# Kernel tuning notes

Measured on AMD Instinct MI355X. Metric: run time of the kernel, lower is better.

The kernel has to match this reference:

```python
import jax, jax.numpy as jnp
import numpy as np

NEG_INF = -1e8  # masked_fill value from the torch code
EPS_DICE = 0.001
EPS_DIV = 1e-5
LOSS_FACTOR = 1.0  # loss['factor']


def conv2d(x, w, b, pad):
    # x: [B,C,H,W], w: [O,I,kh,kw] (OIHW), b: [O]
    y = jax.lax.conv_general_dilated(
        x, w, window_strides=(1, 1), padding=[(pad, pad), (pad, pad)],
        dimension_numbers=("NCHW", "OIHW", "NCHW"))
    return y + b[None, :, None, None]


def setup_inputs() -> dict:
    key = jax.random.key(0)
    ks = jax.random.split(key, 12)
    B, C, H, W = 2, 256, 64, 64
    s = 0.05  # small init scale to keep logits in a sane range
    inp = {
        "feats": jax.random.normal(ks[0], (B, C, H, W), jnp.float32),
        "masks": jax.random.randint(ks[1], (B, H, W), 0, 2).astype(jnp.float32),
        "layouts": jax.random.randint(ks[2], (B, H, W), 0, 16).astype(jnp.int32),
        "w_pre0": jax.random.normal(ks[3], (C, C, 3, 3), jnp.float32) * s,
        "b_pre0": jax.random.normal(ks[4], (C,), jnp.float32) * s,
        "w_pre1": jax.random.normal(ks[5], (C, C, 3, 3), jnp.float32) * s,
        "b_pre1": jax.random.normal(ks[6], (C,), jnp.float32) * s,
        "w_kernel": jax.random.normal(ks[7], (C + 1, C, 1, 1), jnp.float32) * s,
        "b_kernel": jax.random.normal(ks[8], (C + 1,), jnp.float32) * s,
        "w_feats": jax.random.normal(ks[9], (C, C, 1, 1), jnp.float32) * s,
        "b_feats": jax.random.normal(ks[10], (C,), jnp.float32) * s,
    }
    return inp


def reference(feats, masks, layouts, w_pre0, b_pre0, w_pre1, b_pre1,
              w_kernel, b_kernel, w_feats, b_feats):
    B, C, H, W = feats.shape
    # pre_kernel_convs: two 3x3 conv + ReLU
    h = jax.nn.relu(conv2d(feats, w_pre0, b_pre0, pad=1))
    h = jax.nn.relu(conv2d(h, w_pre1, b_pre1, pad=1))
    kernels = conv2d(h, w_kernel, b_kernel, pad=0)          # [B, C+1, H, W]
    f = conv2d(feats, w_feats, b_feats, pad=0)               # [B, C,   H, W]
    # permute(0,2,3,1).reshape(B, H*W, C+1): per-cell dynamic 1x1 conv params
    kernels = kernels.transpose(0, 2, 3, 1).reshape(B, H * W, C + 1)
    kw = kernels[..., :C]                                    # [B, P, C]
    kb = kernels[..., C]                                     # [B, P]
    # grouped 1x1 conv == batched matmul over channel dim
    logits = jnp.einsum("bpc,bchw->bphw", kw, f) + kb[:, :, None, None]
    logits = jnp.where(masks[:, None, :, :] > 0, logits, NEG_INF)  # [B,P,H,W]

    # --- training loss (dice, div='all') ---
    # segm_labels[b, r*W+c] = (layouts[b] == layouts[b,r,c])
    flat = layouts.reshape(B, H * W)
    labels = (layouts[:, None, :, :] == flat[:, :, None, None]).astype(logits.dtype)
    p = jax.nn.sigmoid(logits)
    d = 2.0 * (p * labels) / (p * p + EPS_DICE + labels * labels + EPS_DICE)
    loss_el = 1.0 - d                                        # [B, P, H, W]
    m_flat = masks.reshape(B, H * W)
    num = ((loss_el * masks[:, None, :, :]).sum((-1, -2)) * m_flat).sum(-1)  # [B]
    grid = masks.sum((1, 2))
    loss = (LOSS_FACTOR * num / (grid * grid + EPS_DIV)).mean()
    return logits, loss
```

## Files before the change

kernel.cpp:

```cpp
#include <hip/hip_runtime.h>
#include <hip/hip_bf16.h>
#include <math.h>

typedef __attribute__((ext_vector_type(8))) short bf16x8;
typedef __attribute__((ext_vector_type(4))) float f32x4;
typedef __hip_bfloat16 bf16_t;

#define NEG_INF_V -100000000.0f

__device__ __forceinline__ void gload16(const void* g, void* l) {
  __builtin_amdgcn_global_load_lds(
      (const __attribute__((address_space(1))) unsigned int*)g,
      (__attribute__((address_space(3))) unsigned int*)l, 16, 0, 0);
}

__device__ __forceinline__ bf16x8 swzread(const short* base, int r, int c) {
  return *(const bf16x8*)(base + ((r * 8 + (c ^ (r & 7))) << 3));
}

__global__ __launch_bounds__(256) void pad_cast_k(
    const float* __restrict__ feats, bf16_t* __restrict__ x_pad) {
  __shared__ float s[64][65];
  const int t = threadIdx.x;
  const int y = blockIdx.x, c0 = blockIdx.y * 64, b = blockIdx.z;
  bf16_t* xp = x_pad + (size_t)b * (66 * 66 * 256) + (size_t)y * 66 * 256 + c0;
  if (y == 0 || y == 65) {
    for (int i = t; i < 66 * 64; i += 256) {
      int px = i >> 6, ci = i & 63;
      xp[(size_t)px * 256 + ci] = __float2bfloat16(0.f);
    }
    return;
  }
  const float* fb = feats + ((size_t)b * 256 + c0) * 4096 + (size_t)(y - 1) * 64;
  for (int i = t; i < 64 * 64; i += 256) {
    int ci = i >> 6, x = i & 63;
    s[ci][x] = fb[(size_t)ci * 4096 + x];
  }
  __syncthreads();
  if (t < 128) {
    int px = (t >> 6) * 65, ci = t & 63;
    xp[(size_t)px * 256 + ci] = __float2bfloat16(0.f);
  }
  for (int i = t; i < 64 * 64; i += 256) {
    int xi = i >> 6, ci = i & 63;
    xp[(size_t)(xi + 1) * 256 + ci] = __float2bfloat16(s[ci][xi]);
  }
}

__global__ __launch_bounds__(256) void castw_all_k(
    const float* __restrict__ w0, const float* __restrict__ w1,
    const float* __restrict__ wk, const float* __restrict__ wf,
    bf16_t* __restrict__ o0, bf16_t* __restrict__ o1,
    bf16_t* __restrict__ ok, bf16_t* __restrict__ of) {
  const int bid = blockIdx.x, t = threadIdx.x;
  if (bid < 512) {
    int which = bid >> 8, co = bid & 255;
    const float* ws = which ? w1 : w0;
    bf16_t* wd = which ? o1 : o0;
#pragma unroll
    for (int k = 0; k < 9; ++k)
      wd[(size_t)co * 2304 + k * 256 + t] = __float2bfloat16(ws[((size_t)co * 256 + t) * 9 + k]);
  } else {
    int i = (bid - 512) * 256 + t;
    if (i < 257 * 256) ok[i] = __float2bfloat16(wk[i]);
    else { int j = i - 257 * 256; if (j < 256 * 256) of[j] = __float2bfloat16(wf[j]); }
  }
}

__global__ __launch_bounds__(256) void conv3x3_mfma_k(
    const bf16_t* __restrict__ xpad, const bf16_t* __restrict__ wr,
    const float* __restrict__ bias, bf16_t* __restrict__ out,
    int out_row_stride, int out_base, long out_bstride) {
  __shared__ __align__(16) short ldsA[2][8192];
  __shared__ __align__(16) short ldsB[2][8192];
  const int t = threadIdx.x, w = t >> 6, lane = t & 63;
  const int y = blockIdx.x, co0 = blockIdx.y * 64, b = blockIdx.z;
  const bf16_t* xb = xpad + (size_t)b * (66 * 66 * 256);
  const int wm = w >> 1, wn = w & 1;
  f32x4 acc[2][2] = {};

  int arow[4], akh[4], alsl[4];
#pragma unroll
  for (int pp = 0; pp < 4; ++pp) {
    int u = (pp * 4 + w) * 64 + lane;
    int gr = u >> 3, slot = u & 7;
    arow[pp] = gr & 63; akh[pp] = gr >> 6;
    alsl[pp] = (slot ^ (gr & 7)) * 8;
  }
  const int fr = lane & 15, fc = lane >> 4;

  auto stage = [&](int ks, int buf) {
    int kpos = ks >> 1, ck0 = (ks & 1) * 128;
    int ky = (kpos * 11) >> 5, kx = kpos - 3 * ky;
#pragma unroll
    for (int pp = 0; pp < 4; ++pp) {
      gload16(xb + ((size_t)(y + ky) * 66 + arow[pp] + kx) * 256 + kpos * 0 + ck0 + akh[pp] * 64 + alsl[pp]
                 + (size_t)kpos * 0,
              &ldsA[buf][(pp * 4 + w) * 512]);
      gload16(wr + (size_t)(co0 + arow[pp]) * 2304 + kpos * 256 + ck0 + akh[pp] * 64 + alsl[pp],
              &ldsB[buf][(pp * 4 + w) * 512]);
    }
  };
  auto compute = [&](int buf) {
#pragma unroll
    for (int kk = 0; kk < 4; ++kk) {
      const short* bA = &ldsA[buf][(kk >> 1) * 4096];
      const short* bB = &ldsB[buf][(kk >> 1) * 4096];
      int c = (kk & 1) * 4 + fc;
      bf16x8 af[2], bfr[2];
#pragma unroll
      for (int m = 0; m < 2; ++m) af[m] = swzread(bA, wm * 32 + m * 16 + fr, c);
#pragma unroll
      for (int n = 0; n < 2; ++n) bfr[n] = swzread(bB, wn * 32 + n * 16 + fr, c);
#pragma unroll
      for (int m = 0; m < 2; ++m)
#pragma unroll
        for (int n = 0; n < 2; ++n)
          acc[m][n] = __builtin_amdgcn_mfma_f32_16x16x32_bf16(af[m], bfr[n], acc[m][n], 0, 0, 0);
    }
  };

  stage(0, 0);
  __syncthreads();
  for (int ks = 0; ks < 17; ++ks) {
    stage(ks + 1, (ks + 1) & 1);
    compute(ks & 1);
    __syncthreads();
  }
  compute(1);

  bf16_t* ob = out + (size_t)b * out_bstride;
  float bv[2];
#pragma unroll
  for (int n = 0; n < 2; ++n) bv[n] = bias[co0 + wn * 32 + n * 16 + fr];
#pragma unroll
  for (int m = 0; m < 2; ++m)
#pragma unroll
    for (int r = 0; r < 4; ++r) {
      int x = wm * 32 + m * 16 + fc * 4 + r;
      size_t ra = (size_t)out_base + (size_t)y * out_row_stride + (size_t)x * 256 + co0 + wn * 32 + fr;
#pragma unroll
      for (int n = 0; n < 2; ++n) {
        float v = acc[m][n][r] + bv[n];
        ob[ra + n * 16] = __float2bfloat16(fmaxf(v, 0.f));
      }
    }
}

template <bool KER>
__global__ __launch_bounds__(256) void conv1x1_mfma_k(
    const bf16_t* __restrict__ in, const bf16_t* __restrict__ wt,
    const float* __restrict__ bias, bf16_t* __restrict__ outw,
    float* __restrict__ outkb, int A0, int AS, long in_bstride, int comax) {
  __shared__ __align__(16) short ldsA[16384];
  __shared__ __align__(16) short ldsB[16384];
  const int t = threadIdx.x, w = t >> 6, lane = t & 63;
  const int y = blockIdx.x, co0 = blockIdx.y * 64, b = blockIdx.z;
  const bf16_t* inb = in + (size_t)b * in_bstride;
  const int wm = w >> 1, wn = w & 1;
  f32x4 acc[2][2] = {};
  const int fr = lane & 15, fc = lane >> 4;

#pragma unroll
  for (int pp = 0; pp < 8; ++pp) {
    int u = (pp * 4 + w) * 64 + lane;
    int gr = u >> 3, slot = u & 7;
    int row = gr & 63, kh = gr >> 6;
    int lsl = (slot ^ (gr & 7)) * 8;
    gload16(inb + (size_t)A0 + (size_t)y * AS + (size_t)row * 256 + kh * 64 + lsl,
            &ldsA[(pp * 4 + w) * 512]);
    gload16(wt + (size_t)min(co0 + row, comax - 1) * 256 + kh * 64 + lsl,
            &ldsB[(pp * 4 + w) * 512]);
  }
  __syncthreads();
#pragma unroll
  for (int kk = 0; kk < 8; ++kk) {
    const short* bA = &ldsA[(kk >> 1) * 4096];
    const short* bB = &ldsB[(kk >> 1) * 4096];
    int c = (kk & 1) * 4 + fc;
    bf16x8 af[2], bfr[2];
#pragma unroll
    for (int m = 0; m < 2; ++m) af[m] = swzread(bA, wm * 32 + m * 16 + fr, c);
#pragma unroll
    for (int n = 0; n < 2; ++n) bfr[n] = swzread(bB, wn * 32 + n * 16 + fr, c);
#pragma unroll
    for (int m = 0; m < 2; ++m)
#pragma unroll
      for (int n = 0; n < 2; ++n)
        acc[m][n] = __builtin_amdgcn_mfma_f32_16x16x32_bf16(af[m], bfr[n], acc[m][n], 0, 0, 0);
  }

#pragma unroll
  for (int m = 0; m < 2; ++m)
#pragma unroll
    for (int r = 0; r < 4; ++r) {
      int x = wm * 32 + m * 16 + fc * 4 + r;
      int prow = y * 64 + x;
#pragma unroll
      for (int n = 0; n < 2; ++n) {
        int co = co0 + wn * 32 + n * 16 + fr;
        float v = acc[m][n][r] + bias[min(co, comax - 1)];
        if (KER) {
          if (co < 256) outw[((size_t)b * 4096 + prow) * 256 + co] = __float2bfloat16(v);
          else if (co == 256) outkb[(size_t)b * 4096 + prow] = v;
        } else {
          outw[((size_t)b * 4096 + prow) * 256 + co] = __float2bfloat16(v);
        }
      }
    }
}

__global__ __launch_bounds__(256) void logits_mfma_k(
    const bf16_t* __restrict__ kwt, const float* __restrict__ kb,
    const bf16_t* __restrict__ fft, const float* __restrict__ masks,
    const int* __restrict__ layouts, float* __restrict__ out,
    float* __restrict__ partial) {
  __shared__ __align__(16) short ldsA[2][8192];
  __shared__ __align__(16) short ldsB[2][8192];
  const int t = threadIdx.x, w = t >> 6, lane = t & 63;
  const int p0 = blockIdx.x * 128, q0 = blockIdx.y * 128, b = blockIdx.z;
  const bf16_t* ab = kwt + (size_t)b * (4096 * 256);
  const bf16_t* bb = fft + (size_t)b * (4096 * 256);
  const int wm = w >> 1, wn = w & 1;
  f32x4 acc[4][4] = {};

  int grow[4], glsl[4];
#pragma unroll
  for (int pp = 0; pp < 4; ++pp) {
    int u = (pp * 4 + w) * 64 + lane;
    int gr = u >> 3, slot = u & 7;
    grow[pp] = gr;
    glsl[pp] = (slot ^ (gr & 7)) * 8;
  }
  const int fr = lane & 15, fc = lane >> 4;

  auto stage = [&](int ks, int buf) {
    int cik = ks * 64;
#pragma unroll
    for (int pp = 0; pp < 4; ++pp) {
      gload16(ab + (size_t)(p0 + grow[pp]) * 256 + cik + glsl[pp], &ldsA[buf][(pp * 4 + w) * 512]);
      gload16(bb + (size_t)(q0 + grow[pp]) * 256 + cik + glsl[pp], &ldsB[buf][(pp * 4 + w) * 512]);
    }
  };
  auto compute = [&](int buf) {
#pragma unroll
    for (int kk = 0; kk < 2; ++kk) {
      int c = kk * 4 + fc;
      bf16x8 af[4], bfr[4];
#pragma unroll
      for (int m = 0; m < 4; ++m) af[m] = swzread(ldsA[buf], wm * 64 + m * 16 + fr, c);
#pragma unroll
      for (int n = 0; n < 4; ++n) bfr[n] = swzread(ldsB[buf], wn * 64 + n * 16 + fr, c);
#pragma unroll
      for (int m = 0; m < 4; ++m)
#pragma unroll
        for (int n = 0; n < 4; ++n)
          acc[m][n] = __builtin_amdgcn_mfma_f32_16x16x32_bf16(af[m], bfr[n], acc[m][n], 0, 0, 0);
    }
  };

  stage(0, 0);
  __syncthreads();
  for (int ks = 0; ks < 3; ++ks) {
    stage(ks + 1, (ks + 1) & 1);
    compute(ks & 1);
    __syncthreads();
  }
  compute(1);

  float mq[4];
  int layq[4];
#pragma unroll
  for (int n = 0; n < 4; ++n) {
    int q = q0 + wn * 64 + n * 16 + fr;
    mq[n] = masks[b * 4096 + q];
    layq[n] = layouts[b * 4096 + q];
  }
  float sl[16];
#pragma unroll
  for (int i = 0; i < 16; ++i) sl[i] = 0.f;
  float* outb = out + (size_t)b * 4096 * 4096;
#pragma unroll
  for (int m = 0; m < 4; ++m) {
#pragma unroll
    for (int r = 0; r < 4; ++r) {
      int p = p0 + wm * 64 + m * 16 + fc * 4 + r;
      float kbv = kb[b * 4096 + p];
      int layp = layouts[b * 4096 + p];
      float s = 0.f;
      size_t ra = (size_t)p * 4096 + q0 + wn * 64 + fr;
#pragma unroll
      for (int n = 0; n < 4; ++n) {
        float lg = (mq[n] > 0.f) ? (acc[m][n][r] + kbv) : NEG_INF_V;
        outb[ra + n * 16] = lg;
        float pz = 1.f / (1.f + __expf(-lg));
        float lab = (layp == layq[n]) ? 1.f : 0.f;
        float d = 2.f * pz * lab / (pz * pz + lab + 0.002f);
        s += (1.f - d) * mq[n];
      }
      sl[m * 4 + r] = s;
    }
  }
#pragma unroll
  for (int i = 0; i < 16; ++i) {
    float v = sl[i];
    v += __shfl_xor(v, 1); v += __shfl_xor(v, 2);
    v += __shfl_xor(v, 4); v += __shfl_xor(v, 8);
    sl[i] = v;
  }
  if (fr == 0) {
    int qt = blockIdx.y * 2 + wn;
#pragma unroll
    for (int m = 0; m < 4; ++m)
#pragma unroll
      for (int r = 0; r < 4; ++r) {
        int p = p0 + wm * 64 + m * 16 + fc * 4 + r;
        partial[((size_t)b * 4096 + p) * 64 + qt] = sl[m * 4 + r];
      }
  }
}

__global__ __launch_bounds__(256) void rowsum_k(
    const float* __restrict__ partial, const float* __restrict__ masks,
    float* __restrict__ accum) {
  const int t = threadIdx.x, w = t >> 6, lane = t & 63;
  const int idx = blockIdx.x * 256 + t;
  const int b = idx >> 12;
  const float* pp = partial + (size_t)idx * 64;
  float s = 0.f;
#pragma unroll
  for (int k = 0; k < 64; ++k) s += pp[k];
  float mp = masks[idx];
  float num = s * mp;
#pragma unroll
  for (int off = 32; off; off >>= 1) {
    num += __shfl_down(num, off);
    mp += __shfl_down(mp, off);
  }
  __shared__ float sn[4], sm[4];
  if (lane == 0) { sn[w] = num; sm[w] = mp; }
  __syncthreads();
  if (t == 0) {
    atomicAdd(&accum[b * 2], sn[0] + sn[1] + sn[2] + sn[3]);
    atomicAdd(&accum[b * 2 + 1], sm[0] + sm[1] + sm[2] + sm[3]);
  }
}

__global__ void loss_final_k(const float* __restrict__ accum, float* __restrict__ out_loss) {
  if (threadIdx.x == 0) {
    float l0 = accum[0] / (accum[1] * accum[1] + 1e-5f);
    float l1 = accum[2] / (accum[3] * accum[3] + 1e-5f);
    out_loss[0] = 0.5f * (l0 + l1);
  }
}

extern "C" void kernel_launch(void* const* d_in, const int* in_sizes, int n_in,
                              void* d_out, int out_size, void* d_ws, size_t ws_size,
                              hipStream_t stream) {
  const float* feats = (const float*)d_in[0];
  const float* masks = (const float*)d_in[1];
  const int* layouts = (const int*)d_in[2];
  const float* w_pre0 = (const float*)d_in[3];
  const float* b_pre0 = (const float*)d_in[4];
  const float* w_pre1 = (const float*)d_in[5];
  const float* b_pre1 = (const float*)d_in[6];
  const float* w_kernel = (const float*)d_in[7];
  const float* b_kernel = (const float*)d_in[8];
  const float* w_feats = (const float*)d_in[9];
  const float* b_feats = (const float*)d_in[10];

  bf16_t* x_pad = (bf16_t*)d_ws;
  bf16_t* h1p = x_pad + 2 * 1115136;
  bf16_t* h2 = h1p + 2 * 1115136;
  bf16_t* w0r = h2 + 2 * 1048576;
  bf16_t* w1r = w0r + 589824;
  bf16_t* wkb = w1r + 589824;
  bf16_t* wfb = wkb + 65792;
  bf16_t* kwt = wfb + 65536;
  bf16_t* fft = kwt + 2 * 1048576;
  float* kb = (float*)(fft + 2 * 1048576);
  float* partial = kb + 8192;
  float* accum = partial + 524288;
  float* out = (float*)d_out;

  hipMemsetAsync(h1p, 0, (size_t)2 * 1115136 * sizeof(bf16_t), stream);
  hipMemsetAsync(accum, 0, 4 * sizeof(float), stream);

  pad_cast_k<<<dim3(66, 4, 2), 256, 0, stream>>>(feats, x_pad);
  castw_all_k<<<dim3(1026), 256, 0, stream>>>(w_pre0, w_pre1, w_kernel, w_feats,
                                              w0r, w1r, wkb, wfb);

  conv3x3_mfma_k<<<dim3(64, 4, 2), 256, 0, stream>>>(
      x_pad, w0r, b_pre0, h1p, 66 * 256, 67 * 256, 1115136L);
  conv3x3_mfma_k<<<dim3(64, 4, 2), 256, 0, stream>>>(
      h1p, w1r, b_pre1, h2, 64 * 256, 0, 1048576L);

  conv1x1_mfma_k<true><<<dim3(64, 5, 2), 256, 0, stream>>>(
      h2, wkb, b_kernel, kwt, kb, 0, 16384, 1048576L, 257);
  conv1x1_mfma_k<false><<<dim3(64, 4, 2), 256, 0, stream>>>(
      x_pad, wfb, b_feats, fft, nullptr, 67 * 256, 66 * 256, 1115136L, 256);

  logits_mfma_k<<<dim3(32, 32, 2), 256, 0, stream>>>(
      kwt, kb, fft, masks, layouts, out, partial);

  rowsum_k<<<dim3(32), 256, 0, stream>>>(partial, masks, accum);
  loss_final_k<<<1, 64, 0, stream>>>(accum, out + (size_t)2 * 4096 * 4096);
}
```

Before: 293.6 us.

## Stage logits tile through LDS for coalesced float4 stores and simplify dice math

The logits epilogue now writes each 64x128 half-tile into shared memory, reusing the GEMM staging buffer, and then stores it to global memory as row-contiguous float4 writes instead of scattered 4-byte stores. The dice term is rewritten algebraically: it is computed from exp(-lg) with one reciprocal, only label-matching entries are accumulated, and the row total is mqsum minus that sum. This targets the 134 MB logits output write, which dominates traffic. It adds extra syncthreads and serialises the two warp-row halves, and the exp is clamped to avoid overflow.

```diff
diff --git a/kernel.cpp b/kernel.cpp
--- a/kernel.cpp
+++ b/kernel.cpp
@@ -94,8 +94,7 @@
     int ky = (kpos * 11) >> 5, kx = kpos - 3 * ky;
 #pragma unroll
     for (int pp = 0; pp < 4; ++pp) {
-      gload16(xb + ((size_t)(y + ky) * 66 + arow[pp] + kx) * 256 + kpos * 0 + ck0 + akh[pp] * 64 + alsl[pp]
-                 + (size_t)kpos * 0,
+      gload16(xb + ((size_t)(y + ky) * 66 + arow[pp] + kx) * 256 + ck0 + akh[pp] * 64 + alsl[pp],
               &ldsA[buf][(pp * 4 + w) * 512]);
       gload16(wr + (size_t)(co0 + arow[pp]) * 2304 + kpos * 256 + ck0 + akh[pp] * 64 + alsl[pp],
               &ldsB[buf][(pp * 4 + w) * 512]);
@@ -215,8 +214,10 @@
     const bf16_t* __restrict__ fft, const float* __restrict__ masks,
     const int* __restrict__ layouts, float* __restrict__ out,
     float* __restrict__ partial) {
-  __shared__ __align__(16) short ldsA[2][8192];
-  __shared__ __align__(16) short ldsB[2][8192];
+  __shared__ __align__(16) short ldsbuf[32768];
+  short* ldsA0 = ldsbuf;
+  short* ldsB0 = ldsbuf + 16384;
+  float* ldsf = (float*)ldsbuf;
   const int t = threadIdx.x, w = t >> 6, lane = t & 63;
   const int p0 = blockIdx.x * 128, q0 = blockIdx.y * 128, b = blockIdx.z;
   const bf16_t* ab = kwt + (size_t)b * (4096 * 256);
@@ -238,8 +239,10 @@
     int cik = ks * 64;
 #pragma unroll
     for (int pp = 0; pp < 4; ++pp) {
-      gload16(ab + (size_t)(p0 + grow[pp]) * 256 + cik + glsl[pp], &ldsA[buf][(pp * 4 + w) * 512]);
-      gload16(bb + (size_t)(q0 + grow[pp]) * 256 + cik + glsl[pp], &ldsB[buf][(pp * 4 + w) * 512]);
+      gload16(ab + (size_t)(p0 + grow[pp]) * 256 + cik + glsl[pp],
+              &ldsA0[buf * 8192 + (pp * 4 + w) * 512]);
+      gload16(bb + (size_t)(q0 + grow[pp]) * 256 + cik + glsl[pp],
+              &ldsB0[buf * 8192 + (pp * 4 + w) * 512]);
     }
   };
   auto compute = [&](int buf) {
@@ -248,9 +251,9 @@
       int c = kk * 4 + fc;
       bf16x8 af[4], bfr[4];
 #pragma unroll
-      for (int m = 0; m < 4; ++m) af[m] = swzread(ldsA[buf], wm * 64 + m * 16 + fr, c);
-#pragma unroll
-      for (int n = 0; n < 4; ++n) bfr[n] = swzread(ldsB[buf], wn * 64 + n * 16 + fr, c);
+      for (int m = 0; m < 4; ++m) af[m] = swzread(&ldsA0[buf * 8192], wm * 64 + m * 16 + fr, c);
+#pragma unroll
+      for (int n = 0; n < 4; ++n) bfr[n] = swzread(&ldsB0[buf * 8192], wn * 64 + n * 16 + fr, c);
 #pragma unroll
       for (int m = 0; m < 4; ++m)
 #pragma unroll
@@ -276,31 +279,51 @@
     mq[n] = masks[b * 4096 + q];
     layq[n] = layouts[b * 4096 + q];
   }
+  float mqsum = mq[0] + mq[1] + mq[2] + mq[3];
+  mqsum += __shfl_xor(mqsum, 1); mqsum += __shfl_xor(mqsum, 2);
+  mqsum += __shfl_xor(mqsum, 4); mqsum += __shfl_xor(mqsum, 8);
+
   float sl[16];
-#pragma unroll
-  for (int i = 0; i < 16; ++i) sl[i] = 0.f;
   float* outb = out + (size_t)b * 4096 * 4096;
-#pragma unroll
-  for (int m = 0; m < 4; ++m) {
-#pragma unroll
-    for (int r = 0; r < 4; ++r) {
-      int p = p0 + wm * 64 + m * 16 + fc * 4 + r;
-      float kbv = kb[b * 4096 + p];
-      int layp = layouts[b * 4096 + p];
-      float s = 0.f;
-      size_t ra = (size_t)p * 4096 + q0 + wn * 64 + fr;
-#pragma unroll
-      for (int n = 0; n < 4; ++n) {
-        float lg = (mq[n] > 0.f) ? (acc[m][n][r] + kbv) : NEG_INF_V;
-        outb[ra + n * 16] = lg;
-        float pz = 1.f / (1.f + __expf(-lg));
-        float lab = (layp == layq[n]) ? 1.f : 0.f;
-        float d = 2.f * pz * lab / (pz * pz + lab + 0.002f);
-        s += (1.f - d) * mq[n];
+  __syncthreads();
+
+  for (int half = 0; half < 2; ++half) {
+    if (wm == half) {
+#pragma unroll
+      for (int m = 0; m < 4; ++m) {
+#pragma unroll
+        for (int r = 0; r < 4; ++r) {
+          int pl = m * 16 + fc * 4 + r;
+          int p = p0 + wm * 64 + pl;
+          float kbv = kb[b * 4096 + p];
+          int layp = layouts[b * 4096 + p];
+          float dsum = 0.f;
+#pragma unroll
+          for (int n = 0; n < 4; ++n) {
+            float lg = (mq[n] > 0.f) ? (acc[m][n][r] + kbv) : NEG_INF_V;
+            ldsf[pl * 132 + wn * 64 + n * 16 + fr] = lg;
+            float E = __expf(fminf(-lg, 87.f));
+            float u = 1.f + E;
+            float den = fmaf(1.002f * u, u, 1.f);
+            float d = 2.f * u * __builtin_amdgcn_rcpf(den);
+            dsum += (layp == layq[n]) ? mq[n] * d : 0.f;
+          }
+          sl[m * 4 + r] = dsum;
+        }
       }
-      sl[m * 4 + r] = s;
-    }
-  }
+    }
+    __syncthreads();
+#pragma unroll
+    for (int j = 0; j < 8; ++j) {
+      int row = w * 16 + j * 2 + (lane >> 5);
+      int colf = (lane & 31) * 4;
+      float4 v = *(float4*)&ldsf[row * 132 + colf];
+      int p = p0 + half * 64 + row;
+      *(float4*)&outb[(size_t)p * 4096 + q0 + colf] = v;
+    }
+    __syncthreads();
+  }
+
 #pragma unroll
   for (int i = 0; i < 16; ++i) {
     float v = sl[i];
@@ -315,7 +338,7 @@
 #pragma unroll
       for (int r = 0; r < 4; ++r) {
         int p = p0 + wm * 64 + m * 16 + fc * 4 + r;
-        partial[((size_t)b * 4096 + p) * 64 + qt] = sl[m * 4 + r];
+        partial[((size_t)b * 4096 + p) * 64 + qt] = mqsum - sl[m * 4 + r];
       }
   }
 }
```

After: 268.4 us. 1.09x faster.
